# Kernel tuning notes

Measured on AMD Instinct MI355X. Metric: run time of the kernel, lower is better.

## Reference

```python
import jax, jax.numpy as jnp
import numpy as np

# LightweightConv1d config (matches init_kwargs)
C = 1024        # input_size / channels
H = 16          # num_heads
K = 7           # kernel_size (odd)
PAD = 3         # padding (same-length output)


def setup_inputs() -> dict:
    key = jax.random.key(0)
    kx, kw = jax.random.split(key)
    x = jax.random.normal(kx, (8, 4096, C), dtype=jnp.float32)   # B x T x C
    weight = jax.random.uniform(kw, (H, 1, K), dtype=jnp.float32)  # per-head kernel
    return {"x": x, "weight": weight}


def reference(x, weight):
    # x: (B, T, C); weight: (H, 1, K)
    B, T, _ = x.shape
    # weight softmax over the kernel dimension (weight_softmax=True)
    w = jax.nn.softmax(weight.reshape(H, K), axis=-1)  # (H, K)
    # weight_dropout is identity at inference (eval mode)
    # channel c uses head c % H -> tile head kernels C//H times along channel axis
    w_chan = jnp.tile(w, (C // H, 1))[:, None, :]      # (C, 1, K) depthwise kernel
    x_nct = jnp.transpose(x, (0, 2, 1))                # (B, C, T)
    y = jax.lax.conv_general_dilated(
        x_nct, w_chan,
        window_strides=(1,),
        padding=[(PAD, PAD)],
        dimension_numbers=("NCH", "OIH", "NCH"),
        feature_group_count=C,
    )                                                  # (B, C, T), same length
    return jnp.transpose(y, (0, 2, 1))                 # (B, T, C)
```

## Files before the change

### kernel.cpp

```cpp
#include <hip/hip_runtime.h>


constexpr int B_   = 8;
constexpr int T_   = 4096;
constexpr int C_   = 1024;
constexpr int H_   = 16;
constexpr int K_   = 7;
constexpr int PAD_ = 3;
constexpr int TCHUNK = 16;
constexpr int W_  = TCHUNK + K_ - 1;
constexpr int C4  = C_ / 4;
constexpr int NCHUNK = T_ / TCHUNK;
constexpr int NXCD = 8;

typedef float vfloat4 __attribute__((ext_vector_type(4)));

__global__ __launch_bounds__(256, 3) void lwconv_kernel(
    const float* __restrict__ x, const float* __restrict__ w,
    float* __restrict__ y) {
  __shared__ float ws[H_][K_];
  const int tid = threadIdx.x;

  if (tid < H_) {
    float v[K_];
    float m = -1e30f;
#pragma unroll
    for (int k = 0; k < K_; ++k) { v[k] = w[tid * K_ + k]; m = fmaxf(m, v[k]); }
    float s = 0.f;
#pragma unroll
    for (int k = 0; k < K_; ++k) { v[k] = expf(v[k] - m); s += v[k]; }
    const float inv = 1.f / s;
#pragma unroll
    for (int k = 0; k < K_; ++k) ws[tid][k] = v[k] * inv;
  }
  __syncthreads();

  const int h0 = (4 * tid) & (H_ - 1);
  float wr[4][K_];
#pragma unroll
  for (int j = 0; j < 4; ++j)
#pragma unroll
    for (int k = 0; k < K_; ++k) wr[j][k] = ws[h0 + j][k];

  const int cpx = (B_ * NCHUNK) / NXCD;
  const int wid = ((int)blockIdx.x % NXCD) * cpx + (int)blockIdx.x / NXCD;
  const int b  = wid / NCHUNK;
  const int t0 = (wid % NCHUNK) * TCHUNK;

  const float4* __restrict__ xr =
      reinterpret_cast<const float4*>(x + (size_t)b * T_ * C_) + tid;
  vfloat4* __restrict__ yr =
      reinterpret_cast<vfloat4*>(y + (size_t)b * T_ * C_) + tid;

  const float4 z4 = make_float4(0.f, 0.f, 0.f, 0.f);

  float4 win[W_];
#pragma unroll
  for (int i = 0; i < W_; ++i) {
    const int t = t0 - PAD_ + i;
    win[i] = (t >= 0 && t < T_) ? xr[(size_t)t * C4] : z4;
  }

#pragma unroll
  for (int tt = 0; tt < TCHUNK; ++tt) {
    float ax = 0.f, ay = 0.f, az = 0.f, aw = 0.f;
#pragma unroll
    for (int k = 0; k < K_; ++k) {
      ax = fmaf(win[tt + k].x, wr[0][k], ax);
      ay = fmaf(win[tt + k].y, wr[1][k], ay);
      az = fmaf(win[tt + k].z, wr[2][k], az);
      aw = fmaf(win[tt + k].w, wr[3][k], aw);
    }
    vfloat4 out;
    out.x = ax; out.y = ay; out.z = az; out.w = aw;
    __builtin_nontemporal_store(out, yr + (size_t)(t0 + tt) * C4);
  }
}

extern "C" void kernel_launch(void* const* d_in, const int* in_sizes, int n_in,
                              void* d_out, int out_size, void* d_ws, size_t ws_size,
                              hipStream_t stream) {
  const float* x = (const float*)d_in[0];
  const float* w = (const float*)d_in[1];
  float* y = (float*)d_out;

  const int grid = B_ * NCHUNK;
  lwconv_kernel<<<grid, 256, 0, stream>>>(x, w, y);
}
```

Before: 244.0 us.

## Stream input rows through a register ring buffer over larger time chunks

Each block now covers 32 timesteps instead of 16. It keeps a 16-entry register ring of input rows and issues the load for a future row right after each output is written, so loads run ahead of the FMAs by about ten steps. This cuts the halo re-read overhead per output row and overlaps global loads with compute. Launch bounds rise to 4 blocks per CU to fit the smaller register window. The trade-off is half as many blocks and a longer serial dependency chain inside each thread.

After: 242.0 us. No clear change (-0.8%).

```diff
diff --git a/kernel.cpp b/kernel.cpp
--- a/kernel.cpp
+++ b/kernel.cpp
@@ -7,15 +7,15 @@
 constexpr int H_   = 16;
 constexpr int K_   = 7;
 constexpr int PAD_ = 3;
-constexpr int TCHUNK = 16;
-constexpr int W_  = TCHUNK + K_ - 1;
-constexpr int C4  = C_ / 4;
-constexpr int NCHUNK = T_ / TCHUNK;
+constexpr int BT   = 32;
+constexpr int NB   = 16;
+constexpr int C4   = C_ / 4;
+constexpr int NCHUNK = T_ / BT;
 constexpr int NXCD = 8;
 
 typedef float vfloat4 __attribute__((ext_vector_type(4)));
 
-__global__ __launch_bounds__(256, 3) void lwconv_kernel(
+__global__ __launch_bounds__(256, 4) void lwconv_kernel(
     const float* __restrict__ x, const float* __restrict__ w,
     float* __restrict__ y) {
   __shared__ float ws[H_][K_];
@@ -35,17 +35,17 @@
   }
   __syncthreads();
 
+  const int cpx = (B_ * NCHUNK) / NXCD;
+  const int wid = ((int)blockIdx.x % NXCD) * cpx + (int)blockIdx.x / NXCD;
+  const int b  = wid / NCHUNK;
+  const int t0 = (wid % NCHUNK) * BT;
+
   const int h0 = (4 * tid) & (H_ - 1);
   float wr[4][K_];
 #pragma unroll
   for (int j = 0; j < 4; ++j)
 #pragma unroll
     for (int k = 0; k < K_; ++k) wr[j][k] = ws[h0 + j][k];
-
-  const int cpx = (B_ * NCHUNK) / NXCD;
-  const int wid = ((int)blockIdx.x % NXCD) * cpx + (int)blockIdx.x / NXCD;
-  const int b  = wid / NCHUNK;
-  const int t0 = (wid % NCHUNK) * TCHUNK;
 
   const float4* __restrict__ xr =
       reinterpret_cast<const float4*>(x + (size_t)b * T_ * C_) + tid;
@@ -54,26 +54,32 @@
 
   const float4 z4 = make_float4(0.f, 0.f, 0.f, 0.f);
 
-  float4 win[W_];
+  float4 win[NB];
 #pragma unroll
-  for (int i = 0; i < W_; ++i) {
-    const int t = t0 - PAD_ + i;
-    win[i] = (t >= 0 && t < T_) ? xr[(size_t)t * C4] : z4;
+  for (int s = 0; s < NB; ++s) {
+    const int t = t0 - PAD_ + s;
+    win[s] = (t >= 0) ? xr[(size_t)t * C4] : z4;
   }
 
 #pragma unroll
-  for (int tt = 0; tt < TCHUNK; ++tt) {
+  for (int t = 0; t < BT; ++t) {
     float ax = 0.f, ay = 0.f, az = 0.f, aw = 0.f;
 #pragma unroll
     for (int k = 0; k < K_; ++k) {
-      ax = fmaf(win[tt + k].x, wr[0][k], ax);
-      ay = fmaf(win[tt + k].y, wr[1][k], ay);
-      az = fmaf(win[tt + k].z, wr[2][k], az);
-      aw = fmaf(win[tt + k].w, wr[3][k], aw);
+      const int s = (t + k) & (NB - 1);
+      ax = fmaf(win[s].x, wr[0][k], ax);
+      ay = fmaf(win[s].y, wr[1][k], ay);
+      az = fmaf(win[s].z, wr[2][k], az);
+      aw = fmaf(win[s].w, wr[3][k], aw);
     }
     vfloat4 out;
     out.x = ax; out.y = ay; out.z = az; out.w = aw;
-    __builtin_nontemporal_store(out, yr + (size_t)(t0 + tt) * C4);
+    __builtin_nontemporal_store(out, yr + (size_t)(t0 + t) * C4);
+
+    if (t < BT - 10) {
+      const int tr = t0 + (NB - PAD_) + t;
+      win[t & (NB - 1)] = (tr < T_) ? xr[(size_t)tr * C4] : z4;
+    }
   }
 }
 
```
